# Performance work log

Measured on AMD Instinct MI355X. Metric: run time of the kernel, lower is better.

## Reference

```python
import jax, jax.numpy as jnp
import numpy as np
from jax import lax

EPS = 1e-5

def _conv3x3(x, w, stride=1):
    # x: [B,C,H,W], w: [O,I,3,3]
    dn = lax.conv_dimension_numbers(x.shape, w.shape, ('NCHW', 'OIHW', 'NCHW'))
    return lax.conv_general_dilated(x, w, window_strides=(stride, stride),
                                    padding=((1, 1), (1, 1)), dimension_numbers=dn)

def _batchnorm(x, gamma, beta):
    # training-mode BN over (N,H,W) per channel
    mean = jnp.mean(x, axis=(0, 2, 3), keepdims=True)
    var = jnp.var(x, axis=(0, 2, 3), keepdims=True)
    inv = lax.rsqrt(var + EPS)
    return (x - mean) * inv * gamma[None, :, None, None] + beta[None, :, None, None]

def setup_inputs() -> dict:
    key = jax.random.key(0)
    ks = jax.random.split(key, 8)
    B, C, H, W, E = 16, 256, 64, 64, 512
    x = jax.random.normal(ks[0], (B, C, H, W), dtype=jnp.float32)
    embedding = jax.random.normal(ks[1], (B, E), dtype=jnp.float32)
    s_conv = 1.0 / np.sqrt(C * 9)
    conv1_w = jax.random.normal(ks[2], (C, C, 3, 3), dtype=jnp.float32) * s_conv
    conv2_w = jax.random.normal(ks[3], (C, C, 3, 3), dtype=jnp.float32) * s_conv
    s_g = 1.0 / np.sqrt(E)
    g1_w = jax.random.normal(ks[4], (E, C), dtype=jnp.float32) * s_g
    g1_b = jnp.zeros((C,), dtype=jnp.float32)
    g2_w = jax.random.normal(ks[5], (E, C), dtype=jnp.float32) * s_g
    g2_b = jnp.zeros((C,), dtype=jnp.float32)
    bn1_g = jnp.ones((C,), dtype=jnp.float32)
    bn1_b = jnp.zeros((C,), dtype=jnp.float32)
    bn2_g = jnp.ones((C,), dtype=jnp.float32)
    bn2_b = jnp.zeros((C,), dtype=jnp.float32)
    return {"x": x, "embedding": embedding, "conv1_w": conv1_w, "conv2_w": conv2_w,
            "g1_w": g1_w, "g1_b": g1_b, "g2_w": g2_w, "g2_b": g2_b,
            "bn1_g": bn1_g, "bn1_b": bn1_b, "bn2_g": bn2_g, "bn2_b": bn2_b}

def reference(x, embedding, conv1_w, conv2_w, g1_w, g1_b, g2_w, g2_b,
              bn1_g, bn1_b, bn2_g, bn2_b):
    identity = x
    # gate 1: per-sample per-channel gate values (softmax over channels)
    gate1 = jax.nn.softmax(embedding @ g1_w + g1_b, axis=-1)  # [B,C]
    out = _conv3x3(x, conv1_w, stride=1) * gate1[:, :, None, None]
    out = jax.nn.relu(_batchnorm(out, bn1_g, bn1_b))
    # gate 2
    gate2 = jax.nn.softmax(embedding @ g2_w + g2_b, axis=-1)  # [B,C]
    out = _conv3x3(out, conv2_w, stride=1) * gate2[:, :, None, None]
    out = _batchnorm(out, bn2_g, bn2_b)
    out = jax.nn.relu(out + identity)
    return (out, gate1, gate2)
```

## Files before the change

kernel.cpp:

```cpp
#include <hip/hip_runtime.h>

typedef __attribute__((ext_vector_type(8))) short short8;
typedef __attribute__((ext_vector_type(4))) float f32x4;

#define HP 66

__device__ __forceinline__ unsigned short f2bf(float f) {
  unsigned u = __builtin_bit_cast(unsigned, f);
  u += 0x7FFFu + ((u >> 16) & 1u);
  return (unsigned short)(u >> 16);
}
__device__ __forceinline__ float bf2f(unsigned short h) {
  return __builtin_bit_cast(float, ((unsigned)h) << 16);
}
__device__ __forceinline__ __attribute__((address_space(3))) void* to_as3(void* p) {
  return (__attribute__((address_space(3))) void*)(unsigned)(unsigned long long)p;
}
__device__ __forceinline__ const __attribute__((address_space(1))) void* to_as1(const void* p) {
  return (const __attribute__((address_space(1))) void*)(unsigned long long)p;
}

#define SB0() __builtin_amdgcn_sched_barrier(0)
#define BAR() do { SB0(); __builtin_amdgcn_s_barrier(); SB0(); } while (0)

__global__ void k_halo_zero(unsigned int* xp) {
  int p = blockIdx.x % 260;
  int b = blockIdx.x / 260;
  int h, w;
  if (p < 66)      { h = 0;  w = p; }
  else if (p < 132){ h = 65; w = p - 66; }
  else             { int q = p - 132; h = 1 + (q >> 1); w = (q & 1) * 65; }
  unsigned int* dst = xp + ((long)((b*HP + h)*HP + w) * 256) / 2;
  dst[threadIdx.x] = 0u;
  dst[threadIdx.x + 64] = 0u;
}

__global__ __launch_bounds__(256) void k_convert_x(const float* __restrict__ x,
                                                   unsigned short* __restrict__ xp) {
  __shared__ float tile[32][65];
  int blk = blockIdx.x;
  int ct = blk & 7, h = (blk >> 3) & 63, b = blk >> 9;
  int c0 = ct * 32;
  int t = threadIdx.x;
  int w = t & 63, cs = t >> 6;
#pragma unroll
  for (int i = 0; i < 8; ++i) {
    int c = cs + i * 4;
    tile[c][w] = x[(((b * 256) + c0 + c) * 64 + h) * 64 + w];
  }
  __syncthreads();
  int cl = (t & 15) * 2, w0 = t >> 4;
#pragma unroll
  for (int i = 0; i < 4; ++i) {
    int ww = w0 + i * 16;
    unsigned v = (unsigned)f2bf(tile[cl][ww]) | ((unsigned)f2bf(tile[cl + 1][ww]) << 16);
    *(unsigned*)(xp + ((long)((b*HP + h + 1)*HP + (ww + 1)) * 256 + c0 + cl)) = v;
  }
}

__global__ void k_pack_w(const float* __restrict__ w1, const float* __restrict__ w2,
                         unsigned short* __restrict__ wT1, unsigned short* __restrict__ wT2) {
  const float* w = blockIdx.y ? w2 : w1;
  unsigned short* wT = blockIdx.y ? wT2 : wT1;
  int co = blockIdx.x;
  int t = threadIdx.x;
#pragma unroll
  for (int kk = 0; kk < 9; ++kk) {
    wT[co * 2304 + kk * 256 + t] = f2bf(w[(co * 256 + t) * 9 + kk]);
  }
}

__global__ __launch_bounds__(256) void k_gates(const float* __restrict__ emb,
                                               const float* __restrict__ g1w,
                                               const float* __restrict__ g1b,
                                               const float* __restrict__ g2w,
                                               const float* __restrict__ g2b,
                                               float* __restrict__ gate1,
                                               float* __restrict__ gate2) {
  const float* gw = blockIdx.y ? g2w : g1w;
  const float* gbias = blockIdx.y ? g2b : g1b;
  float* gout = blockIdx.y ? gate2 : gate1;
  __shared__ float ebuf[512];
  __shared__ float red[8];
  int b = blockIdx.x, t = threadIdx.x;
  ebuf[t] = emb[b * 512 + t];
  ebuf[t + 256] = emb[b * 512 + t + 256];
  __syncthreads();
  float acc = gbias[t];
  for (int k = 0; k < 512; ++k) acc += ebuf[k] * gw[k * 256 + t];
  float mx = acc;
  for (int off = 32; off >= 1; off >>= 1) mx = fmaxf(mx, __shfl_xor(mx, off));
  if ((t & 63) == 0) red[t >> 6] = mx;
  __syncthreads();
  mx = fmaxf(fmaxf(red[0], red[1]), fmaxf(red[2], red[3]));
  float e = expf(acc - mx);
  float sm = e;
  for (int off = 32; off >= 1; off >>= 1) sm += __shfl_xor(sm, off);
  if ((t & 63) == 0) red[4 + (t >> 6)] = sm;
  __syncthreads();
  sm = red[4] + red[5] + red[6] + red[7];
  gout[b * 256 + t] = e / sm;
}

__global__ __launch_bounds__(512, 2) void k_conv(
    const unsigned short* __restrict__ inp,
    const unsigned short* __restrict__ wT,
    const float* __restrict__ gate,
    unsigned short* __restrict__ yout,
    float* __restrict__ partials) {
  __shared__ short As[2][256][64];
  __shared__ short Bs[2][256][64];
  __shared__ float sbuf[2][256][2];

  const int t = threadIdx.x;
  const int lane = t & 63;
  const int wid = t >> 6;
  const int wm = wid >> 2;
  const int wn = wid & 3;
  const int lr = lane & 15;
  const int hi = lane >> 4;
  const int key = lr & 7;

  const int blk = ((blockIdx.x & 7) << 5) + (blockIdx.x >> 3);
  const int b = blk >> 4;
  const int hh4 = (blk & 15) << 2;

  const int r0 = t >> 3;
  const int cdst = (t & 7) << 3;
  const int cg8 = (((t & 7) ^ ((t >> 3) & 7)) << 3);

  int aoff[4];
#pragma unroll
  for (int i = 0; i < 4; ++i)
    aoff[i] = (b * HP + hh4 + i) * HP + r0;

  auto stageA = [&](int buf, int half, int s) {
    int kk = s >> 2;
    int kh = (kk * 11) >> 5;
    int khw = kh * 66 + (kk - kh * 3);
    int ci = ((s & 3) << 6) + cg8;
    const unsigned short* g0 = inp + (long)(aoff[half * 2 + 0] + khw) * 256 + ci;
    const unsigned short* g1 = inp + (long)(aoff[half * 2 + 1] + khw) * 256 + ci;
    __builtin_amdgcn_global_load_lds(to_as1(g0), to_as3((void*)&As[buf][half * 128 + r0][cdst]), 16, 0, 0);
    __builtin_amdgcn_global_load_lds(to_as1(g1), to_as3((void*)&As[buf][half * 128 + 64 + r0][cdst]), 16, 0, 0);
  };
  auto stageB = [&](int buf, int half, int s) {
    int co0 = half * 128 + r0;
    const unsigned short* g0 = wT + (long)co0 * 2304 + s * 64 + cg8;
    const unsigned short* g1 = wT + (long)(co0 + 64) * 2304 + s * 64 + cg8;
    __builtin_amdgcn_global_load_lds(to_as1(g0), to_as3((void*)&Bs[buf][half * 128 + r0][cdst]), 16, 0, 0);
    __builtin_amdgcn_global_load_lds(to_as1(g1), to_as3((void*)&Bs[buf][half * 128 + 64 + r0][cdst]), 16, 0, 0);
  };

  f32x4 acc[8][4];
#pragma unroll
  for (int i = 0; i < 8; ++i)
#pragma unroll
    for (int j = 0; j < 4; ++j) acc[i][j] = (f32x4){0.f, 0.f, 0.f, 0.f};

  stageA(0, 0, 0); stageA(0, 1, 0); stageB(0, 0, 0); stageB(0, 1, 0);
  stageA(1, 0, 1); stageA(1, 1, 1); stageB(1, 0, 1);
  asm volatile("s_waitcnt vmcnt(6)" ::: "memory");
  BAR();

  short8 afrag[8][2], bfrag[4][2];

#define QUAD2(mh, nh)                                                                \
  do {                                                                               \
    __builtin_amdgcn_s_setprio(1);                                                   \
    _Pragma("unroll") for (int ks = 0; ks < 2; ++ks)                                 \
      _Pragma("unroll") for (int mo = 0; mo < 4; ++mo)                               \
        _Pragma("unroll") for (int no = 0; no < 2; ++no)                             \
          acc[(mh) * 4 + mo][(nh) * 2 + no] = __builtin_amdgcn_mfma_f32_16x16x32_bf16( \
              afrag[(mh) * 4 + mo][ks], bfrag[(nh) * 2 + no][ks],                    \
              acc[(mh) * 4 + mo][(nh) * 2 + no], 0, 0, 0);                           \
    __builtin_amdgcn_s_setprio(0);                                                   \
  } while (0)

  for (int kt = 0; kt < 36; ++kt) {
    const int cur = kt & 1;
#pragma unroll
    for (int nf = 0; nf < 2; ++nf)
#pragma unroll
      for (int ks = 0; ks < 2; ++ks)
        bfrag[nf][ks] = *(const short8*)&Bs[cur][wn * 64 + nf * 16 + lr][((ks * 4 + hi) ^ key) << 3];
#pragma unroll
    for (int mf = 0; mf < 4; ++mf)
#pragma unroll
      for (int ks = 0; ks < 2; ++ks)
        afrag[mf][ks] = *(const short8*)&As[cur][wm * 128 + mf * 16 + lr][((ks * 4 + hi) ^ key) << 3];
    if (kt + 1 < 36) stageB(cur ^ 1, 1, kt + 1);
    BAR();
    QUAD2(0, 0);
    BAR();
#pragma unroll
    for (int nf = 2; nf < 4; ++nf)
#pragma unroll
      for (int ks = 0; ks < 2; ++ks)
        bfrag[nf][ks] = *(const short8*)&Bs[cur][wn * 64 + nf * 16 + lr][((ks * 4 + hi) ^ key) << 3];
#pragma unroll
    for (int mf = 4; mf < 8; ++mf)
#pragma unroll
      for (int ks = 0; ks < 2; ++ks)
        afrag[mf][ks] = *(const short8*)&As[cur][wm * 128 + mf * 16 + lr][((ks * 4 + hi) ^ key) << 3];
    BAR();
    QUAD2(1, 1);
    asm volatile("s_waitcnt lgkmcnt(0)" ::: "memory");
    BAR();
    if (kt + 2 < 36) stageA(cur, 0, kt + 2);
    BAR();
    QUAD2(0, 1);
    BAR();
    if (kt + 2 < 36) { stageA(cur, 1, kt + 2); stageB(cur, 0, kt + 2); }
    BAR();
    QUAD2(1, 0);
    if (kt < 34) asm volatile("s_waitcnt vmcnt(6)" ::: "memory");
    else         asm volatile("s_waitcnt vmcnt(0)" ::: "memory");
    BAR();
  }
#undef QUAD2

  float g[4];
#pragma unroll
  for (int nf = 0; nf < 4; ++nf) g[nf] = gate[(b << 8) + wn * 64 + nf * 16 + lr];

  float s[4] = {0, 0, 0, 0}, sq[4] = {0, 0, 0, 0};
  const int mrow0 = (blk << 8) + wm * 128 + (hi << 2);
  const int c0 = wn * 64 + lr;
#pragma unroll
  for (int mf = 0; mf < 8; ++mf)
#pragma unroll
    for (int r = 0; r < 4; ++r) {
      const int mm = mrow0 + mf * 16 + r;
#pragma unroll
      for (int nf = 0; nf < 4; ++nf) {
        float v = acc[mf][nf][r] * g[nf];
        yout[(long)mm * 256 + c0 + nf * 16] = f2bf(v);
        s[nf] += v;
        sq[nf] += v * v;
      }
    }
#pragma unroll
  for (int nf = 0; nf < 4; ++nf) {
    s[nf] += __shfl_xor(s[nf], 16);  s[nf] += __shfl_xor(s[nf], 32);
    sq[nf] += __shfl_xor(sq[nf], 16); sq[nf] += __shfl_xor(sq[nf], 32);
  }
  if (hi == 0) {
#pragma unroll
    for (int nf = 0; nf < 4; ++nf) {
      int c = wn * 64 + nf * 16 + lr;
      sbuf[wm][c][0] = s[nf];
      sbuf[wm][c][1] = sq[nf];
    }
  }
  __syncthreads();
  if (t < 256) {
    partials[((blk << 8) + t) * 2]     = sbuf[0][t][0] + sbuf[1][t][0];
    partials[((blk << 8) + t) * 2 + 1] = sbuf[0][t][1] + sbuf[1][t][1];
  }
}

__global__ __launch_bounds__(256) void k_bnfin(const float* __restrict__ partials,
                                               const float* __restrict__ gamma,
                                               const float* __restrict__ beta,
                                               float2* __restrict__ aff) {
  __shared__ float red[8];
  int c = blockIdx.x, t = threadIdx.x;
  float s = partials[(t * 256 + c) * 2];
  float sq = partials[(t * 256 + c) * 2 + 1];
  for (int off = 32; off >= 1; off >>= 1) { s += __shfl_xor(s, off); sq += __shfl_xor(sq, off); }
  if ((t & 63) == 0) { red[t >> 6] = s; red[4 + (t >> 6)] = sq; }
  __syncthreads();
  if (t == 0) {
    s = red[0] + red[1] + red[2] + red[3];
    sq = red[4] + red[5] + red[6] + red[7];
    float mean = s * (1.0f / 65536.0f);
    float var = fmaxf(sq * (1.0f / 65536.0f) - mean * mean, 0.0f);
    float inv = rsqrtf(var + 1e-5f);
    float ga = gamma[c] * inv;
    aff[c] = make_float2(ga, beta[c] - mean * ga);
  }
}

__global__ __launch_bounds__(256) void k_mid(const unsigned short* __restrict__ y1,
                                             const float2* __restrict__ aff,
                                             unsigned short* __restrict__ zp) {
  long idx = (long)blockIdx.x * 256 + threadIdx.x;
  int c0 = (int)(idx & 31) * 8;
  long pos = idx >> 5;
  int b = (int)(pos >> 12), hw = (int)(pos & 4095);
  int h = hw >> 6, w = hw & 63;
  uint4 v = *(const uint4*)(y1 + pos * 256 + c0);
  unsigned vv[4] = {v.x, v.y, v.z, v.w};
  unsigned outp[4];
#pragma unroll
  for (int j = 0; j < 4; ++j) {
    float2 aL = aff[c0 + 2 * j], aH = aff[c0 + 2 * j + 1];
    float lo = fmaxf(aL.x * bf2f((unsigned short)(vv[j] & 0xFFFF)) + aL.y, 0.f);
    float hiv = fmaxf(aH.x * bf2f((unsigned short)(vv[j] >> 16)) + aH.y, 0.f);
    outp[j] = (unsigned)f2bf(lo) | ((unsigned)f2bf(hiv) << 16);
  }
  unsigned short* dst = zp + (long)((b * HP + h + 1) * HP + w + 1) * 256 + c0;
  *(uint4*)dst = make_uint4(outp[0], outp[1], outp[2], outp[3]);
}

__global__ __launch_bounds__(256) void k_final(const unsigned short* __restrict__ y2,
                                               const float2* __restrict__ aff,
                                               const float* __restrict__ x,
                                               float* __restrict__ out) {
  __shared__ float tile[64][33];
  int blk = blockIdx.x;
  int ct = blk & 7, h = (blk >> 3) & 63, b = blk >> 9;
  int c0 = ct * 32;
  int t = threadIdx.x;
  int cl = (t & 15) * 2, w0 = t >> 4;
#pragma unroll
  for (int i = 0; i < 4; ++i) {
    int w = w0 + i * 16;
    unsigned v = *(const unsigned*)(y2 + (long)((b * 4096) + h * 64 + w) * 256 + c0 + cl);
    float2 aL = aff[c0 + cl], aH = aff[c0 + cl + 1];
    tile[w][cl] = aL.x * bf2f((unsigned short)(v & 0xFFFF)) + aL.y;
    tile[w][cl + 1] = aH.x * bf2f((unsigned short)(v >> 16)) + aH.y;
  }
  __syncthreads();
  int w = t & 63, csub = t >> 6;
#pragma unroll
  for (int j = 0; j < 8; ++j) {
    int c = c0 + csub * 8 + j;
    long o = ((long)(b * 256 + c) * 64 + h) * 64 + w;
    out[o] = fmaxf(tile[w][csub * 8 + j] + x[o], 0.f);
  }
}

extern "C" void kernel_launch(void* const* d_in, const int* in_sizes, int n_in,
                              void* d_out, int out_size, void* d_ws, size_t ws_size,
                              hipStream_t stream) {
  const float* x    = (const float*)d_in[0];
  const float* emb  = (const float*)d_in[1];
  const float* w1   = (const float*)d_in[2];
  const float* w2   = (const float*)d_in[3];
  const float* g1w  = (const float*)d_in[4];
  const float* g1b  = (const float*)d_in[5];
  const float* g2w  = (const float*)d_in[6];
  const float* g2b  = (const float*)d_in[7];
  const float* bn1g = (const float*)d_in[8];
  const float* bn1b = (const float*)d_in[9];
  const float* bn2g = (const float*)d_in[10];
  const float* bn2b = (const float*)d_in[11];

  float* out = (float*)d_out;
  float* gate1 = out + 16777216;
  float* gate2 = gate1 + 4096;

  char* ws = (char*)d_ws;
  const size_t OFF_XP  = 0;
  const size_t OFF_WT1 = 35684352;
  const size_t OFF_WT2 = OFF_WT1 + 1179648;
  const size_t OFF_Y   = OFF_WT2 + 1179648;
  const size_t OFF_PART = OFF_Y + 33554432;
  const size_t OFF_AFF1 = OFF_PART + 1048576;
  const size_t OFF_AFF2 = OFF_AFF1 + 2048;

  unsigned short* xp  = (unsigned short*)(ws + OFF_XP);
  unsigned short* wT1 = (unsigned short*)(ws + OFF_WT1);
  unsigned short* wT2 = (unsigned short*)(ws + OFF_WT2);
  unsigned short* y   = (unsigned short*)(ws + OFF_Y);
  float* part = (float*)(ws + OFF_PART);
  float2* aff1 = (float2*)(ws + OFF_AFF1);
  float2* aff2 = (float2*)(ws + OFF_AFF2);

  k_halo_zero<<<16 * 260, 64, 0, stream>>>((unsigned int*)xp);
  k_convert_x<<<8192, 256, 0, stream>>>(x, xp);
  k_pack_w<<<dim3(256, 2), 256, 0, stream>>>(w1, w2, wT1, wT2);
  k_gates<<<dim3(16, 2), 256, 0, stream>>>(emb, g1w, g1b, g2w, g2b, gate1, gate2);

  k_conv<<<256, 512, 0, stream>>>(xp, wT1, gate1, y, part);
  k_bnfin<<<256, 256, 0, stream>>>(part, bn1g, bn1b, aff1);
  k_mid<<<8192, 256, 0, stream>>>(y, aff1, xp);

  k_conv<<<256, 512, 0, stream>>>(xp, wT2, gate2, y, part);
  k_bnfin<<<256, 256, 0, stream>>>(part, bn2g, bn2b, aff2);
  k_final<<<8192, 256, 0, stream>>>(y, aff2, x, out);
}
```

Baseline: 230.3 us.

## Software-pipeline the MFMA loop by deferring second-half quads to next k-tile

The 3x3 conv GEMM main loop is restructured so the two MFMA quadrants that use the second half of the A fragments run during the next k-iteration. Their B fragments are kept in a double-buffered register array, and the loop is unrolled by two so the buffer selector is static. The aim is to overlap LDS fragment reads for the next tile with MFMA work from the previous one and cut stalls between barriers. Doubling the B fragment registers raises VGPR pressure, which risks spills or lower occupancy.

Measured after the change: 292.4 us. 27.0% more time.

```diff
diff --git a/kernel.cpp b/kernel.cpp
--- a/kernel.cpp
+++ b/kernel.cpp
@@ -163,62 +163,74 @@
   asm volatile("s_waitcnt vmcnt(6)" ::: "memory");
   BAR();
 
-  short8 afrag[8][2], bfrag[4][2];
-
-#define QUAD2(mh, nh)                                                                \
+  short8 afrag[8][2];
+  short8 bfrag[2][4][2];
+
+#define QUADX(mh, nh, SEL)                                                           \
   do {                                                                               \
     __builtin_amdgcn_s_setprio(1);                                                   \
     _Pragma("unroll") for (int ks = 0; ks < 2; ++ks)                                 \
       _Pragma("unroll") for (int mo = 0; mo < 4; ++mo)                               \
         _Pragma("unroll") for (int no = 0; no < 2; ++no)                             \
           acc[(mh) * 4 + mo][(nh) * 2 + no] = __builtin_amdgcn_mfma_f32_16x16x32_bf16( \
-              afrag[(mh) * 4 + mo][ks], bfrag[(nh) * 2 + no][ks],                    \
+              afrag[(mh) * 4 + mo][ks], bfrag[SEL][(nh) * 2 + no][ks],               \
               acc[(mh) * 4 + mo][(nh) * 2 + no], 0, 0, 0);                           \
     __builtin_amdgcn_s_setprio(0);                                                   \
   } while (0)
 
-  for (int kt = 0; kt < 36; ++kt) {
-    const int cur = kt & 1;
-#pragma unroll
-    for (int nf = 0; nf < 2; ++nf)
-#pragma unroll
-      for (int ks = 0; ks < 2; ++ks)
-        bfrag[nf][ks] = *(const short8*)&Bs[cur][wn * 64 + nf * 16 + lr][((ks * 4 + hi) ^ key) << 3];
-#pragma unroll
-    for (int mf = 0; mf < 4; ++mf)
-#pragma unroll
-      for (int ks = 0; ks < 2; ++ks)
-        afrag[mf][ks] = *(const short8*)&As[cur][wm * 128 + mf * 16 + lr][((ks * 4 + hi) ^ key) << 3];
-    if (kt + 1 < 36) stageB(cur ^ 1, 1, kt + 1);
-    BAR();
-    QUAD2(0, 0);
-    BAR();
-#pragma unroll
-    for (int nf = 2; nf < 4; ++nf)
-#pragma unroll
-      for (int ks = 0; ks < 2; ++ks)
-        bfrag[nf][ks] = *(const short8*)&Bs[cur][wn * 64 + nf * 16 + lr][((ks * 4 + hi) ^ key) << 3];
-#pragma unroll
-    for (int mf = 4; mf < 8; ++mf)
-#pragma unroll
-      for (int ks = 0; ks < 2; ++ks)
-        afrag[mf][ks] = *(const short8*)&As[cur][wm * 128 + mf * 16 + lr][((ks * 4 + hi) ^ key) << 3];
-    BAR();
-    QUAD2(1, 1);
-    asm volatile("s_waitcnt lgkmcnt(0)" ::: "memory");
-    BAR();
-    if (kt + 2 < 36) stageA(cur, 0, kt + 2);
-    BAR();
-    QUAD2(0, 1);
-    BAR();
-    if (kt + 2 < 36) { stageA(cur, 1, kt + 2); stageB(cur, 0, kt + 2); }
-    BAR();
-    QUAD2(1, 0);
-    if (kt < 34) asm volatile("s_waitcnt vmcnt(6)" ::: "memory");
-    else         asm volatile("s_waitcnt vmcnt(0)" ::: "memory");
-    BAR();
-  }
-#undef QUAD2
+#define READS_B(SEL)                                                                 \
+  _Pragma("unroll") for (int nf = 0; nf < 4; ++nf)                                   \
+    _Pragma("unroll") for (int ks = 0; ks < 2; ++ks)                                 \
+      bfrag[SEL][nf][ks] =                                                           \
+          *(const short8*)&Bs[SEL][wn * 64 + nf * 16 + lr][((ks * 4 + hi) ^ key) << 3];
+
+#define READS_A(SEL, MH)                                                             \
+  _Pragma("unroll") for (int mf = 0; mf < 4; ++mf)                                   \
+    _Pragma("unroll") for (int ks = 0; ks < 2; ++ks)                                 \
+      afrag[(MH) * 4 + mf][ks] =                                                     \
+          *(const short8*)&As[SEL][wm * 128 + ((MH) * 4 + mf) * 16 + lr][((ks * 4 + hi) ^ key) << 3];
+
+#define KTBODY(kt, SEL)                                                              \
+  {                                                                                  \
+                                                                             \
+    READS_B(SEL);                                                                    \
+    if ((kt) + 1 < 36) stageB((SEL) ^ 1, 1, (kt) + 1);                               \
+    BAR();                                                                           \
+    if ((kt) > 0) QUADX(1, 1, (SEL) ^ 1);                                            \
+    BAR();                                                                           \
+                                                                             \
+    READS_A(SEL, 0);                                                                 \
+    BAR();                                                                           \
+    if ((kt) > 0) QUADX(1, 0, (SEL) ^ 1);                                            \
+    BAR();                                                                           \
+                                                                             \
+    READS_A(SEL, 1);                                                                 \
+    BAR();                                                                           \
+    QUADX(0, 0, SEL);                                                                \
+    asm volatile("s_waitcnt lgkmcnt(0)" ::: "memory");                               \
+    SB0();                                                                           \
+    BAR();                                                                           \
+                                                                             \
+    if ((kt) + 2 < 36) { stageA(SEL, 0, (kt) + 2); stageA(SEL, 1, (kt) + 2); stageB(SEL, 0, (kt) + 2); } \
+    BAR();                                                                           \
+    QUADX(0, 1, SEL);                                                                \
+    if ((kt) < 34) { asm volatile("s_waitcnt vmcnt(6)" ::: "memory"); }              \
+    else           { asm volatile("s_waitcnt vmcnt(0)" ::: "memory"); }              \
+    SB0();                                                                           \
+    BAR();                                                                           \
+  }
+
+  for (int i = 0; i < 18; ++i) {
+    const int kt0 = 2 * i;
+    KTBODY(kt0, 0);
+    KTBODY(kt0 + 1, 1);
+  }
+  QUADX(1, 1, 1);
+  QUADX(1, 0, 1);
+#undef KTBODY
+#undef READS_A
+#undef READS_B
+#undef QUADX
 
   float g[4];
 #pragma unroll
```

## Software-pipeline LDS fragment reads across quadrants with double register sets

Applied to the files above, without the earlier changes.

Splits the A/B fragment registers into two half-sets and reorders the four MFMA quadrants so that each quadrant's LDS reads overlap the previous quadrant's MFMAs. The first fragments of the next K-tile are prefetched during the last quadrant. Global-to-LDS staging is reshuffled to match, with new vmcnt thresholds. The aim is to hide LDS read latency and cut barrier stalls. The fixed vmcnt counts in the tail iterations, where fewer loads are issued, may wait too little, which risks reading incomplete LDS data.

After: 228.4 us. No clear change (-0.8%).

```diff
diff --git a/kernel.cpp b/kernel.cpp
--- a/kernel.cpp
+++ b/kernel.cpp
@@ -158,67 +158,66 @@
 #pragma unroll
     for (int j = 0; j < 4; ++j) acc[i][j] = (f32x4){0.f, 0.f, 0.f, 0.f};
 
-  stageA(0, 0, 0); stageA(0, 1, 0); stageB(0, 0, 0); stageB(0, 1, 0);
-  stageA(1, 0, 1); stageA(1, 1, 1); stageB(1, 0, 1);
-  asm volatile("s_waitcnt vmcnt(6)" ::: "memory");
-  BAR();
-
-  short8 afrag[8][2], bfrag[4][2];
-
-#define QUAD2(mh, nh)                                                                \
+  short8 afrag0[4][2], afrag1[4][2];
+  short8 bfrag0[2][2], bfrag1[2][2];
+
+#define RD_A(ARR, MH, BUF)                                                           \
+  _Pragma("unroll") for (int mf = 0; mf < 4; ++mf)                                   \
+    _Pragma("unroll") for (int ks = 0; ks < 2; ++ks)                                 \
+      ARR[mf][ks] = *(const short8*)&As[BUF][wm * 128 + ((MH) * 4 + mf) * 16 + lr][((ks * 4 + hi) ^ key) << 3];
+#define RD_B(ARR, NH, BUF)                                                           \
+  _Pragma("unroll") for (int nf = 0; nf < 2; ++nf)                                   \
+    _Pragma("unroll") for (int ks = 0; ks < 2; ++ks)                                 \
+      ARR[nf][ks] = *(const short8*)&Bs[BUF][wn * 64 + ((NH) * 2 + nf) * 16 + lr][((ks * 4 + hi) ^ key) << 3];
+
+#define QUADQ(AF, BF, mh, nh)                                                        \
   do {                                                                               \
     __builtin_amdgcn_s_setprio(1);                                                   \
     _Pragma("unroll") for (int ks = 0; ks < 2; ++ks)                                 \
       _Pragma("unroll") for (int mo = 0; mo < 4; ++mo)                               \
         _Pragma("unroll") for (int no = 0; no < 2; ++no)                             \
           acc[(mh) * 4 + mo][(nh) * 2 + no] = __builtin_amdgcn_mfma_f32_16x16x32_bf16( \
-              afrag[(mh) * 4 + mo][ks], bfrag[(nh) * 2 + no][ks],                    \
-              acc[(mh) * 4 + mo][(nh) * 2 + no], 0, 0, 0);                           \
+              AF[mo][ks], BF[no][ks], acc[(mh) * 4 + mo][(nh) * 2 + no], 0, 0, 0);   \
     __builtin_amdgcn_s_setprio(0);                                                   \
   } while (0)
 
+  stageA(0, 0, 0); stageB(0, 0, 0); stageB(0, 1, 0); stageA(0, 1, 0);
+  stageA(1, 0, 1); stageB(1, 0, 1); stageB(1, 1, 1); stageA(1, 1, 1);
+  asm volatile("s_waitcnt vmcnt(12)" ::: "memory");
+  BAR();
+  RD_B(bfrag0, 0, 0);
+  RD_A(afrag0, 0, 0);
+  asm volatile("s_waitcnt vmcnt(10)" ::: "memory");
+  BAR();
+
   for (int kt = 0; kt < 36; ++kt) {
     const int cur = kt & 1;
-#pragma unroll
-    for (int nf = 0; nf < 2; ++nf)
-#pragma unroll
-      for (int ks = 0; ks < 2; ++ks)
-        bfrag[nf][ks] = *(const short8*)&Bs[cur][wn * 64 + nf * 16 + lr][((ks * 4 + hi) ^ key) << 3];
-#pragma unroll
-    for (int mf = 0; mf < 4; ++mf)
-#pragma unroll
-      for (int ks = 0; ks < 2; ++ks)
-        afrag[mf][ks] = *(const short8*)&As[cur][wm * 128 + mf * 16 + lr][((ks * 4 + hi) ^ key) << 3];
-    if (kt + 1 < 36) stageB(cur ^ 1, 1, kt + 1);
-    BAR();
-    QUAD2(0, 0);
-    BAR();
-#pragma unroll
-    for (int nf = 2; nf < 4; ++nf)
-#pragma unroll
-      for (int ks = 0; ks < 2; ++ks)
-        bfrag[nf][ks] = *(const short8*)&Bs[cur][wn * 64 + nf * 16 + lr][((ks * 4 + hi) ^ key) << 3];
-#pragma unroll
-    for (int mf = 4; mf < 8; ++mf)
-#pragma unroll
-      for (int ks = 0; ks < 2; ++ks)
-        afrag[mf][ks] = *(const short8*)&As[cur][wm * 128 + mf * 16 + lr][((ks * 4 + hi) ^ key) << 3];
-    BAR();
-    QUAD2(1, 1);
-    asm volatile("s_waitcnt lgkmcnt(0)" ::: "memory");
-    BAR();
-    if (kt + 2 < 36) stageA(cur, 0, kt + 2);
-    BAR();
-    QUAD2(0, 1);
-    BAR();
-    if (kt + 2 < 36) { stageA(cur, 1, kt + 2); stageB(cur, 0, kt + 2); }
-    BAR();
-    QUAD2(1, 0);
-    if (kt < 34) asm volatile("s_waitcnt vmcnt(6)" ::: "memory");
-    else         asm volatile("s_waitcnt vmcnt(0)" ::: "memory");
-    BAR();
-  }
-#undef QUAD2
+    const int nxt = cur ^ 1;
+    RD_B(bfrag1, 1, cur);
+    BAR();
+    QUADQ(afrag0, bfrag0, 0, 0);
+    asm volatile("s_waitcnt vmcnt(8)" ::: "memory");
+    BAR();
+    RD_A(afrag1, 1, cur);
+    if (kt + 2 < 36) { stageA(cur, 0, kt + 2); stageB(cur, 0, kt + 2); }
+    BAR();
+    QUADQ(afrag0, bfrag1, 0, 1);
+    BAR();
+    if (kt + 2 < 36) stageB(cur, 1, kt + 2);
+    BAR();
+    QUADQ(afrag1, bfrag0, 1, 0);
+    asm volatile("s_waitcnt vmcnt(10)" ::: "memory");
+    BAR();
+    if (kt < 35) { RD_B(bfrag0, 0, nxt); RD_A(afrag0, 0, nxt); }
+    if (kt + 2 < 36) stageA(cur, 1, kt + 2);
+    BAR();
+    QUADQ(afrag1, bfrag1, 1, 1);
+    asm volatile("s_waitcnt vmcnt(10)" ::: "memory");
+    BAR();
+  }
+#undef QUADQ
+#undef RD_A
+#undef RD_B
 
   float g[4];
 #pragma unroll
```
